# Performance work log

Hardware: AMD Instinct MI355X
Metric: run time of the kernel (lower is better)

## Reference

```python
import jax, jax.numpy as jnp
import numpy as np

TAU = 2.0        # BrainCog LIFNode default tau
THRESHOLD = 1.0
V_RESET = 0.0
HID = 512
OUT = 7
T = 16

@jax.custom_vjp
def spike(v):
    # Heaviside forward, arctan surrogate backward (BrainCog-style surrogate grad)
    return (v > 0).astype(v.dtype)

def _spike_fwd(v):
    return spike(v), v

def _spike_bwd(v, g):
    alpha = 2.0
    sg = (alpha / 2.0) / (1.0 + (jnp.pi / 2.0 * alpha * v) ** 2)
    return (g * sg,)

spike.defvjp(_spike_fwd, _spike_bwd)

def lif(mem, inp):
    # v_{t} = v_{t-1} + (I - v_{t-1}) / tau ; hard reset to v_reset=0 on spike
    v = mem + (inp - mem) / TAU
    s = spike(v - THRESHOLD)
    mem_new = v * (1.0 - jax.lax.stop_gradient(s))  # reset uses detached spike
    return mem_new, s

def setup_inputs() -> dict:
    key = jax.random.key(0)
    ks = jax.random.split(key, 9)
    B, D = 16384, 512
    sc = 0.02
    return {
        "x":     jax.random.normal(ks[0], (T, B, D), dtype=jnp.float32),
        "W_gc":  jax.random.normal(ks[1], (D, HID), dtype=jnp.float32) * sc,
        "b_gc":  jnp.zeros((HID,), jnp.float32),
        "W_pc":  jax.random.normal(ks[2], (HID, HID), dtype=jnp.float32) * sc,
        "b_pc":  jnp.zeros((HID,), jnp.float32),
        "W_d1":  jax.random.normal(ks[3], (D + HID, HID), dtype=jnp.float32) * sc,
        "b_d1":  jnp.zeros((HID,), jnp.float32),
        "W_d2":  jax.random.normal(ks[4], (HID, OUT), dtype=jnp.float32) * sc,
        "b_d2":  jnp.zeros((OUT,), jnp.float32),
    }

def reference(x, W_gc, b_gc, W_pc, b_pc, W_d1, b_d1, W_d2, b_d2):
    B = x.shape[1]
    z = jnp.zeros((B, HID), x.dtype)

    def step(carry, xt):
        m1, m2, m3 = carry
        m1, gc = lif(m1, xt @ W_gc + b_gc)                       # gc_layer
        m2, pc = lif(m2, gc @ W_pc + b_pc)                       # pc_layer
        dcn_in = jnp.concatenate([xt, pc], axis=-1)              # [B, 1024]
        m3, s3 = lif(m3, dcn_in @ W_d1 + b_d1)                   # dcn hidden LIF
        out = s3 @ W_d2 + b_d2                                   # [B, 7]
        return (m1, m2, m3), out

    _, outs = jax.lax.scan(step, (z, z, z), x)   # outs: [T, B, 7]
    return jnp.sum(outs, axis=0) / T
```

## Files before the change

### kernel.cpp

```cpp
#include <hip/hip_runtime.h>

#define TT 16
#define DD 512
#define HIDN 512
#define OUTN 7
#define NTOT 1024
#define R2 8

typedef __attribute__((ext_vector_type(8))) _Float16 half8;
typedef __attribute__((ext_vector_type(4))) _Float16 half4;
typedef __attribute__((ext_vector_type(4))) float f32x4;

#define GLD_LDS(g, l) __builtin_amdgcn_global_load_lds(                     \
    (const __attribute__((address_space(1))) void*)(g),                     \
    (__attribute__((address_space(3))) void*)(l), 16, 0, 0)

__global__ void pack_w(const float* __restrict__ Wgc, const float* __restrict__ Wd1,
                       _Float16* __restrict__ Whi, _Float16* __restrict__ Wlo)
{
    const int cell = blockIdx.x * blockDim.x + threadIdx.x;
    const int lane = cell & 63;
    const int ks   = (cell >> 6) & 15;
    const int ct   = cell >> 10;
    const float* W = (ct < 32) ? Wgc : Wd1;
    const int col  = ((ct < 32) ? ct : ct - 32) * 16 + (lane & 15);
    const int k0   = ks * 32 + ((lane >> 4) << 3);
    half8 vh, vl;
#pragma unroll
    for (int j = 0; j < 8; ++j) {
        const float w = W[(size_t)(k0 + j) * HIDN + col];
        const _Float16 h = (_Float16)w;
        vh[j] = h;
        vl[j] = (_Float16)(w - (float)h);
    }
    *reinterpret_cast<half8*>(Whi + (size_t)cell * 8) = vh;
    *reinterpret_cast<half8*>(Wlo + (size_t)cell * 8) = vl;
}

__global__ __launch_bounds__(256, 2)
void gemm_pre(const float* __restrict__ x,
              const _Float16* __restrict__ Whi, const _Float16* __restrict__ Wlo,
              float* __restrict__ G, int B, int c0, int chb)
{
    __shared__ __align__(16) _Float16 Ah[2][4096];
    __shared__ __align__(16) _Float16 Al[2][4096];
    __shared__ __align__(16) _Float16 Bh[2][4096];
    __shared__ __align__(16) _Float16 Bl[2][4096];

    const int tid  = threadIdx.x;
    const int lane = tid & 63;
    const int wave = tid >> 6;
    const int wr   = wave >> 1;
    const int wc   = wave & 1;
    const int t    = blockIdx.z;
    const size_t mrow = (size_t)blockIdx.y * 128;
    const int ct0 = blockIdx.x * 8;

    const float* xb = x + ((size_t)t * B + (size_t)c0 + mrow) * DD;
    float* Gb = G + ((size_t)t * chb + mrow) * NTOT;

    f32x4 acc[4][4];
#pragma unroll
    for (int g = 0; g < 4; ++g)
#pragma unroll
        for (int c = 0; c < 4; ++c) acc[g][c] = (f32x4){0.f, 0.f, 0.f, 0.f};

    float4 ar[4];
    const int row_u0 = tid >> 3;
    const int fg = tid & 7;

#define LOAD_A(kc)                                                            \
    {                                                                         \
        _Pragma("unroll")                                                     \
        for (int u = 0; u < 4; ++u)                                           \
            ar[u] = *reinterpret_cast<const float4*>(                         \
                xb + (size_t)(row_u0 + u * 32) * DD + (kc) * 32 + (fg << 2)); \
    }

#define CVT_WRITE(BUF)                                                        \
    {                                                                         \
        _Pragma("unroll")                                                     \
        for (int u = 0; u < 4; ++u) {                                         \
            const int row = row_u0 + u * 32;                                  \
            const int gg = row >> 4;                                          \
            const int ld = (row & 15) | ((fg >> 1) << 4);                     \
            const int offs = ((gg << 6) + ld) * 8 + ((fg & 1) << 2);          \
            const float fv[4] = {ar[u].x, ar[u].y, ar[u].z, ar[u].w};         \
            half4 vh, vl;                                                     \
            _Pragma("unroll")                                                 \
            for (int j = 0; j < 4; ++j) {                                     \
                const _Float16 h = (_Float16)fv[j];                           \
                vh[j] = h; vl[j] = (_Float16)(fv[j] - (float)h);              \
            }                                                                 \
            *reinterpret_cast<half4*>(&Ah[BUF][offs]) = vh;                   \
            *reinterpret_cast<half4*>(&Al[BUF][offs]) = vl;                   \
        }                                                                     \
    }

#define STAGE_B(kc, BUF)                                                      \
    {                                                                         \
        const int cga = wave << 1, cgb = cga + 1;                             \
        const size_t sa = ((size_t)((ct0 + cga) * 16 + (kc)) * 64 + lane) * 8;\
        const size_t sb = ((size_t)((ct0 + cgb) * 16 + (kc)) * 64 + lane) * 8;\
        GLD_LDS(Whi + sa, &Bh[BUF][cga << 9]);                                \
        GLD_LDS(Wlo + sa, &Bl[BUF][cga << 9]);                                \
        GLD_LDS(Whi + sb, &Bh[BUF][cgb << 9]);                                \
        GLD_LDS(Wlo + sb, &Bl[BUF][cgb << 9]);                                \
    }

#define COMPUTE(BUF)                                                          \
    {                                                                         \
        half8 af[4], alf[4];                                                  \
        _Pragma("unroll")                                                     \
        for (int g = 0; g < 4; ++g) {                                         \
            const int o = (((wr << 2) + g) * 64 + lane) * 8;                  \
            af[g]  = *reinterpret_cast<const half8*>(&Ah[BUF][o]);            \
            alf[g] = *reinterpret_cast<const half8*>(&Al[BUF][o]);            \
        }                                                                     \
        _Pragma("unroll")                                                     \
        for (int c = 0; c < 4; ++c) {                                         \
            const int o = (((wc << 2) + c) * 64 + lane) * 8;                  \
            const half8 bf  = *reinterpret_cast<const half8*>(&Bh[BUF][o]);   \
            const half8 blf = *reinterpret_cast<const half8*>(&Bl[BUF][o]);   \
            _Pragma("unroll")                                                 \
            for (int g = 0; g < 4; ++g) {                                     \
                acc[g][c] = __builtin_amdgcn_mfma_f32_16x16x32_f16(af[g],  bf,  acc[g][c], 0, 0, 0); \
                acc[g][c] = __builtin_amdgcn_mfma_f32_16x16x32_f16(alf[g], bf,  acc[g][c], 0, 0, 0); \
                acc[g][c] = __builtin_amdgcn_mfma_f32_16x16x32_f16(af[g],  blf, acc[g][c], 0, 0, 0); \
            }                                                                 \
        }                                                                     \
    }

    LOAD_A(0);
    STAGE_B(0, 0);
    CVT_WRITE(0);
    LOAD_A(1);
    __syncthreads();

#pragma unroll 1
    for (int kh = 0; kh < 8; ++kh) {
        CVT_WRITE(1);
        STAGE_B(2 * kh + 1, 1);
        if (2 * kh + 2 < 16) LOAD_A(2 * kh + 2);
        COMPUTE(0);
        __syncthreads();
        if (2 * kh + 2 < 16) {
            CVT_WRITE(0);
            STAGE_B(2 * kh + 2, 0);
        }
        if (2 * kh + 3 < 16) LOAD_A(2 * kh + 3);
        COMPUTE(1);
        __syncthreads();
    }

    const int r0 = (lane >> 4) << 2;
    const int cl = lane & 15;
#pragma unroll
    for (int g = 0; g < 4; ++g)
#pragma unroll
        for (int c = 0; c < 4; ++c) {
            float* gp = Gb + (size_t)((wr << 6) + (g << 4) + r0) * NTOT
                           + (blockIdx.x << 7) + (wc << 6) + (c << 4) + cl;
#pragma unroll
            for (int j = 0; j < 4; ++j) gp[(size_t)j * NTOT] = acc[g][c][j];
        }
#undef LOAD_A
#undef CVT_WRITE
#undef STAGE_B
#undef COMPUTE
}

__global__ __launch_bounds__(256, 4)
void snn_recur(const float* __restrict__ G, const float* __restrict__ bgc,
               const float* __restrict__ Wpc, const float* __restrict__ bpc,
               const float* __restrict__ Wd1, const float* __restrict__ bd1p,
               const float* __restrict__ Wd2, const float* __restrict__ bd2,
               float* __restrict__ out, int c0, int chb)
{
    __shared__ unsigned long long bits1[R2][8];
    __shared__ unsigned long long bits2[R2][8];
    __shared__ unsigned long long bits3[R2][8];
    __shared__ unsigned int rowflag[3];

    const int tid  = threadIdx.x;
    const int lane = tid & 63;
    const int wave = tid >> 6;
    const int row0l = blockIdx.x * R2;

    float m1a[R2], m1b[R2], m2a[R2], m2b[R2], m3a[R2], m3b[R2];
#pragma unroll
    for (int r = 0; r < R2; ++r) {
        m1a[r] = 0.f; m1b[r] = 0.f; m2a[r] = 0.f;
        m2b[r] = 0.f; m3a[r] = 0.f; m3b[r] = 0.f;
    }

    const float bg0 = bgc[tid],  bg1 = bgc[tid + 256];
    const float bp0 = bpc[tid],  bp1 = bpc[tid + 256];
    const float bd0 = bd1p[tid], bd1v = bd1p[tid + 256];

    float out_acc = 0.f;
    const int orow = tid / OUTN;
    const int ocol = tid - orow * OUTN;
    const bool owrite = (tid < R2 * OUTN);

    if (tid < 3) rowflag[tid] = 0u;
    __syncthreads();

#pragma unroll 1
    for (int t = 0; t < TT; ++t) {
        const float* Gt = G + ((size_t)t * chb + row0l) * NTOT;
        float ga[R2], gb[R2], g2[R2], g3[R2];
#pragma unroll
        for (int r = 0; r < R2; ++r) {
            const float* gp = Gt + (size_t)r * NTOT + tid;
            ga[r] = gp[0]; gb[r] = gp[256]; g2[r] = gp[512]; g3[r] = gp[768];
        }

#pragma unroll
        for (int r = 0; r < R2; ++r) {
            const float v0 = m1a[r] + ((ga[r] + bg0) - m1a[r]) * 0.5f;
            const bool s0 = (v0 - 1.0f) > 0.0f;
            m1a[r] = s0 ? 0.0f : v0;
            const unsigned long long k0 = __ballot(s0);
            const float v1 = m1b[r] + ((gb[r] + bg1) - m1b[r]) * 0.5f;
            const bool s1 = (v1 - 1.0f) > 0.0f;
            m1b[r] = s1 ? 0.0f : v1;
            const unsigned long long k1 = __ballot(s1);
            if (lane == 0) {
                bits1[r][wave] = k0; bits1[r][4 + wave] = k1;
                if (k0 | k1) atomicOr(&rowflag[0], 1u << r);
            }
        }
        __syncthreads();
        if (tid == 0) rowflag[2] = 0u;

        {
            const unsigned int rf = rowflag[0];
#pragma unroll
            for (int r = 0; r < R2; ++r) {
                float p0 = bp0, p1 = bp1;
                if (rf & (1u << r)) {
#pragma unroll 1
                    for (int w = 0; w < 8; ++w) {
                        unsigned long long mm = bits1[r][w];
                        while (mm) {
                            const int b = __builtin_ctzll(mm); mm &= (mm - 1);
                            const float* wp = Wpc + (size_t)((w << 6) + b) * HIDN + tid;
                            p0 += wp[0]; p1 += wp[256];
                        }
                    }
                }
                const float v0 = m2a[r] + (p0 - m2a[r]) * 0.5f;
                const bool s0 = (v0 - 1.0f) > 0.0f;
                m2a[r] = s0 ? 0.0f : v0;
                const unsigned long long k0 = __ballot(s0);
                const float v1 = m2b[r] + (p1 - m2b[r]) * 0.5f;
                const bool s1 = (v1 - 1.0f) > 0.0f;
                m2b[r] = s1 ? 0.0f : v1;
                const unsigned long long k1 = __ballot(s1);
                if (lane == 0) {
                    bits2[r][wave] = k0; bits2[r][4 + wave] = k1;
                    if (k0 | k1) atomicOr(&rowflag[1], 1u << r);
                }
            }
        }
        __syncthreads();
        if (tid == 0) rowflag[0] = 0u;

        {
            const unsigned int rf = rowflag[1];
#pragma unroll
            for (int r = 0; r < R2; ++r) {
                float p0 = g2[r] + bd0, p1 = g3[r] + bd1v;
                if (rf & (1u << r)) {
#pragma unroll 1
                    for (int w = 0; w < 8; ++w) {
                        unsigned long long mm = bits2[r][w];
                        while (mm) {
                            const int b = __builtin_ctzll(mm); mm &= (mm - 1);
                            const float* wp = Wd1 + (size_t)(DD + (w << 6) + b) * HIDN + tid;
                            p0 += wp[0]; p1 += wp[256];
                        }
                    }
                }
                const float v0 = m3a[r] + (p0 - m3a[r]) * 0.5f;
                const bool s0 = (v0 - 1.0f) > 0.0f;
                m3a[r] = s0 ? 0.0f : v0;
                const unsigned long long k0 = __ballot(s0);
                const float v1 = m3b[r] + (p1 - m3b[r]) * 0.5f;
                const bool s1 = (v1 - 1.0f) > 0.0f;
                m3b[r] = s1 ? 0.0f : v1;
                const unsigned long long k1 = __ballot(s1);
                if (lane == 0) {
                    bits3[r][wave] = k0; bits3[r][4 + wave] = k1;
                    if (k0 | k1) atomicOr(&rowflag[2], 1u << r);
                }
            }
        }
        __syncthreads();
        if (tid == 0) rowflag[1] = 0u;

        {
            const unsigned int rf = rowflag[2];
            if (owrite && (rf & (1u << orow))) {
#pragma unroll 1
                for (int w = 0; w < 8; ++w) {
                    unsigned long long mm = bits3[orow][w];
                    while (mm) {
                        const int b = __builtin_ctzll(mm); mm &= (mm - 1);
                        out_acc += Wd2[(size_t)((w << 6) + b) * OUTN + ocol];
                    }
                }
            }
        }
    }

    if (owrite)
        out[((size_t)c0 + row0l + orow) * OUTN + ocol] = out_acc * 0.0625f + bd2[ocol];
}

__global__ __launch_bounds__(256, 2)
void snn_fused_fb(const float* __restrict__ x,
                  const float* __restrict__ Wgc, const float* __restrict__ bgc,
                  const float* __restrict__ Wpc, const float* __restrict__ bpc,
                  const float* __restrict__ Wd1, const float* __restrict__ bd1p,
                  const float* __restrict__ Wd2, const float* __restrict__ bd2,
                  float* __restrict__ out, int B)
{
    __shared__ float xs[16 * DD];
    __shared__ unsigned long long bits1[16][8];
    __shared__ unsigned long long bits2[16][8];
    __shared__ unsigned long long bits3[16][8];
    __shared__ unsigned int rowflag[3];

    const int tid  = threadIdx.x;
    const int lane = tid & 63;
    const int wave = tid >> 6;
    const size_t row0 = (size_t)blockIdx.x * 16;

    float m1a[16], m1b[16], m2a[16], m2b[16], m3a[16], m3b[16];
#pragma unroll
    for (int r = 0; r < 16; ++r) {
        m1a[r] = 0.f; m1b[r] = 0.f; m2a[r] = 0.f;
        m2b[r] = 0.f; m3a[r] = 0.f; m3b[r] = 0.f;
    }

    const float bg0 = bgc[tid],  bg1 = bgc[tid + 256];
    const float bp0 = bpc[tid],  bp1 = bpc[tid + 256];
    const float bd0 = bd1p[tid], bd1 = bd1p[tid + 256];

    float out_acc = 0.f;
    const int orow = tid / OUTN;
    const int ocol = tid - orow * OUTN;
    const bool owrite = (tid < 16 * OUTN);

    if (tid < 3) rowflag[tid] = 0;
    {
        const float* src = x + row0 * DD;
#pragma unroll
        for (int u = 0; u < 8; ++u)
            GLD_LDS(src + ((u * 256 + tid) << 2), xs + ((u * 256 + wave * 64) << 2));
    }
    __syncthreads();

    for (int t = 0; t < TT; ++t) {
        float a0[16], a1[16], a2[16], a3[16];
#pragma unroll
        for (int r = 0; r < 16; ++r) { a0[r] = 0.f; a1[r] = 0.f; a2[r] = 0.f; a3[r] = 0.f; }

        const float* gp = Wgc + tid;
        const float* dp = Wd1 + tid;

        float wA0[4], wA1[4], wA2[4], wA3[4];
        float wB0[4], wB1[4], wB2[4], wB3[4];
#pragma unroll
        for (int u = 0; u < 4; ++u) {
            const size_t o = (size_t)u * HIDN;
            wA0[u] = gp[o]; wA1[u] = gp[o + 256];
            wA2[u] = dp[o]; wA3[u] = dp[o + 256];
        }
#pragma unroll 1
        for (int kk = 0; kk < DD; kk += 8) {
#pragma unroll
            for (int u = 0; u < 4; ++u) {
                const size_t o = (size_t)(kk + 4 + u) * HIDN;
                wB0[u] = gp[o]; wB1[u] = gp[o + 256];
                wB2[u] = dp[o]; wB3[u] = dp[o + 256];
            }
#pragma unroll
            for (int r = 0; r < 16; ++r) {
                const float4 xv = *reinterpret_cast<const float4*>(&xs[r * DD + kk]);
                a0[r] = fmaf(xv.x, wA0[0], a0[r]); a0[r] = fmaf(xv.y, wA0[1], a0[r]);
                a0[r] = fmaf(xv.z, wA0[2], a0[r]); a0[r] = fmaf(xv.w, wA0[3], a0[r]);
                a1[r] = fmaf(xv.x, wA1[0], a1[r]); a1[r] = fmaf(xv.y, wA1[1], a1[r]);
                a1[r] = fmaf(xv.z, wA1[2], a1[r]); a1[r] = fmaf(xv.w, wA1[3], a1[r]);
                a2[r] = fmaf(xv.x, wA2[0], a2[r]); a2[r] = fmaf(xv.y, wA2[1], a2[r]);
                a2[r] = fmaf(xv.z, wA2[2], a2[r]); a2[r] = fmaf(xv.w, wA2[3], a2[r]);
                a3[r] = fmaf(xv.x, wA3[0], a3[r]); a3[r] = fmaf(xv.y, wA3[1], a3[r]);
                a3[r] = fmaf(xv.z, wA3[2], a3[r]); a3[r] = fmaf(xv.w, wA3[3], a3[r]);
            }
            const int k2 = (kk + 8) & (DD - 1);
#pragma unroll
            for (int u = 0; u < 4; ++u) {
                const size_t o = (size_t)(k2 + u) * HIDN;
                wA0[u] = gp[o]; wA1[u] = gp[o + 256];
                wA2[u] = dp[o]; wA3[u] = dp[o + 256];
            }
#pragma unroll
            for (int r = 0; r < 16; ++r) {
                const float4 xv = *reinterpret_cast<const float4*>(&xs[r * DD + kk + 4]);
                a0[r] = fmaf(xv.x, wB0[0], a0[r]); a0[r] = fmaf(xv.y, wB0[1], a0[r]);
                a0[r] = fmaf(xv.z, wB0[2], a0[r]); a0[r] = fmaf(xv.w, wB0[3], a0[r]);
                a1[r] = fmaf(xv.x, wB1[0], a1[r]); a1[r] = fmaf(xv.y, wB1[1], a1[r]);
                a1[r] = fmaf(xv.z, wB1[2], a1[r]); a1[r] = fmaf(xv.w, wB1[3], a1[r]);
                a2[r] = fmaf(xv.x, wB2[0], a2[r]); a2[r] = fmaf(xv.y, wB2[1], a2[r]);
                a2[r] = fmaf(xv.z, wB2[2], a2[r]); a2[r] = fmaf(xv.w, wB2[3], a2[r]);
                a3[r] = fmaf(xv.x, wB3[0], a3[r]); a3[r] = fmaf(xv.y, wB3[1], a3[r]);
                a3[r] = fmaf(xv.z, wB3[2], a3[r]); a3[r] = fmaf(xv.w, wB3[3], a3[r]);
            }
        }

#pragma unroll
        for (int r = 0; r < 16; ++r) {
            const float v0 = m1a[r] + ((a0[r] + bg0) - m1a[r]) * 0.5f;
            const bool s0 = (v0 - 1.0f) > 0.0f;
            m1a[r] = s0 ? 0.0f : v0;
            const unsigned long long k0 = __ballot(s0);
            const float v1 = m1b[r] + ((a1[r] + bg1) - m1b[r]) * 0.5f;
            const bool s1 = (v1 - 1.0f) > 0.0f;
            m1b[r] = s1 ? 0.0f : v1;
            const unsigned long long k1 = __ballot(s1);
            if (lane == 0) {
                bits1[r][wave] = k0; bits1[r][4 + wave] = k1;
                if (k0 | k1) atomicOr(&rowflag[0], 1u << r);
            }
        }
        __syncthreads();

        if (tid == 0) rowflag[2] = 0;
        if (t + 1 < TT) {
            const float* src = x + (((size_t)(t + 1) * B) + row0) * DD;
#pragma unroll
            for (int u = 0; u < 8; ++u)
                GLD_LDS(src + ((u * 256 + tid) << 2), xs + ((u * 256 + wave * 64) << 2));
        }

        {
            const unsigned int rf = rowflag[0];
#pragma unroll 1
            for (int r = 0; r < 16; ++r) {
                float p0 = bp0, p1 = bp1;
                if (rf & (1u << r)) {
#pragma unroll 1
                    for (int w = 0; w < 8; ++w) {
                        unsigned long long m = bits1[r][w];
                        while (m) {
                            const int b = __builtin_ctzll(m); m &= (m - 1);
                            const float* wp = Wpc + (size_t)((w << 6) + b) * HIDN + tid;
                            p0 += wp[0]; p1 += wp[256];
                        }
                    }
                }
                const float v0 = m2a[r] + (p0 - m2a[r]) * 0.5f;
                const bool s0 = (v0 - 1.0f) > 0.0f;
                m2a[r] = s0 ? 0.0f : v0;
                const unsigned long long k0 = __ballot(s0);
                const float v1 = m2b[r] + (p1 - m2b[r]) * 0.5f;
                const bool s1 = (v1 - 1.0f) > 0.0f;
                m2b[r] = s1 ? 0.0f : v1;
                const unsigned long long k1 = __ballot(s1);
                if (lane == 0) {
                    bits2[r][wave] = k0; bits2[r][4 + wave] = k1;
                    if (k0 | k1) atomicOr(&rowflag[1], 1u << r);
                }
            }
        }
        __syncthreads();

        if (tid == 0) rowflag[0] = 0;

        {
            const unsigned int rf = rowflag[1];
#pragma unroll 1
            for (int r = 0; r < 16; ++r) {
                float p0 = a2[r] + bd0, p1 = a3[r] + bd1;
                if (rf & (1u << r)) {
#pragma unroll 1
                    for (int w = 0; w < 8; ++w) {
                        unsigned long long m = bits2[r][w];
                        while (m) {
                            const int b = __builtin_ctzll(m); m &= (m - 1);
                            const float* wp = Wd1 + (size_t)(DD + (w << 6) + b) * HIDN + tid;
                            p0 += wp[0]; p1 += wp[256];
                        }
                    }
                }
                const float v0 = m3a[r] + (p0 - m3a[r]) * 0.5f;
                const bool s0 = (v0 - 1.0f) > 0.0f;
                m3a[r] = s0 ? 0.0f : v0;
                const unsigned long long k0 = __ballot(s0);
                const float v1 = m3b[r] + (p1 - m3b[r]) * 0.5f;
                const bool s1 = (v1 - 1.0f) > 0.0f;
                m3b[r] = s1 ? 0.0f : v1;
                const unsigned long long k1 = __ballot(s1);
                if (lane == 0) {
                    bits3[r][wave] = k0; bits3[r][4 + wave] = k1;
                    if (k0 | k1) atomicOr(&rowflag[2], 1u << r);
                }
            }
        }
        __syncthreads();

        if (tid == 0) rowflag[1] = 0;

        {
            const unsigned int rf = rowflag[2];
            if (owrite && (rf & (1u << orow))) {
#pragma unroll 1
                for (int w = 0; w < 8; ++w) {
                    unsigned long long m = bits3[orow][w];
                    while (m) {
                        const int b = __builtin_ctzll(m); m &= (m - 1);
                        out_acc += Wd2[(size_t)((w << 6) + b) * OUTN + ocol];
                    }
                }
            }
        }
    }

    if (owrite) out[(row0 + orow) * OUTN + ocol] = out_acc * 0.0625f + bd2[ocol];
}

extern "C" void kernel_launch(void* const* d_in, const int* in_sizes, int n_in,
                              void* d_out, int out_size, void* d_ws, size_t ws_size,
                              hipStream_t stream) {
    const float* x   = (const float*)d_in[0];
    const float* Wgc = (const float*)d_in[1];
    const float* bgc = (const float*)d_in[2];
    const float* Wpc = (const float*)d_in[3];
    const float* bpc = (const float*)d_in[4];
    const float* Wd1 = (const float*)d_in[5];
    const float* bd1 = (const float*)d_in[6];
    const float* Wd2 = (const float*)d_in[7];
    const float* bd2 = (const float*)d_in[8];
    const int B = in_sizes[0] / (TT * DD);

    const size_t wbytes = (size_t)2 << 20;
    int chb = 4096;
    while (chb > 128 &&
           (wbytes + (size_t)TT * chb * NTOT * 4 > ws_size || (B % chb) != 0))
        chb >>= 1;
    const bool twophase =
        d_ws != nullptr &&
        ws_size >= wbytes + (size_t)TT * chb * NTOT * 4 &&
        (B % chb) == 0 && chb >= 128;

    if (!twophase) {
        hipLaunchKernelGGL(snn_fused_fb, dim3(B / 16), dim3(256), 0, stream,
                           x, Wgc, bgc, Wpc, bpc, Wd1, bd1, Wd2, bd2,
                           (float*)d_out, B);
        return;
    }

    _Float16* Whi = reinterpret_cast<_Float16*>(d_ws);
    _Float16* Wlo = Whi + 64 * 16 * 64 * 8;
    float* G = reinterpret_cast<float*>((char*)d_ws + wbytes);

    hipLaunchKernelGGL(pack_w, dim3(256), dim3(256), 0, stream, Wgc, Wd1, Whi, Wlo);

    for (int c = 0; c < B; c += chb) {
        hipLaunchKernelGGL(gemm_pre, dim3(8, chb / 128, TT), dim3(256), 0, stream,
                           x, Whi, Wlo, G, B, c, chb);
        hipLaunchKernelGGL(snn_recur, dim3(chb / R2), dim3(256), 0, stream,
                           G, bgc, Wpc, bpc, Wd1, bd1, Wd2, bd2,
                           (float*)d_out, c, chb);
    }
}
```

Before: 1.924 ms.

## Prepack x into split-fp16 MFMA layout and stream GEMM operands via global_load_lds

Adds a pack_x kernel that converts x once into hi/lo fp16 tiles already laid out for the MFMA fragments. The GEMM then stages both A and B straight into LDS with global_load_lds, so the per-tile fp32 register loads and in-kernel conversion go away. The batch-chunk loop is dropped in favour of one GEMM and one recurrence launch over the whole batch. The GEMM uses an XCD-aware 1D block mapping and nontemporal stores for G. In exchange it needs a larger workspace for the packed x and the full G, plus an extra pass over x.

```diff
diff --git a/kernel.cpp b/kernel.cpp
--- a/kernel.cpp
+++ b/kernel.cpp
@@ -8,7 +8,6 @@
 #define R2 8
 
 typedef __attribute__((ext_vector_type(8))) _Float16 half8;
-typedef __attribute__((ext_vector_type(4))) _Float16 half4;
 typedef __attribute__((ext_vector_type(4))) float f32x4;
 
 #define GLD_LDS(g, l) __builtin_amdgcn_global_load_lds(                     \
@@ -37,10 +36,45 @@
     *reinterpret_cast<half8*>(Wlo + (size_t)cell * 8) = vl;
 }
 
+__global__ void pack_x(const float* __restrict__ x,
+                       _Float16* __restrict__ Xh, _Float16* __restrict__ Xl)
+{
+    __shared__ float xs[16 * 516];
+    const int tid = threadIdx.x;
+    const size_t sub = blockIdx.x;
+    const float* src = x + sub * (16 * DD);
+#pragma unroll
+    for (int u = 0; u < 8; ++u) {
+        const int f = (u << 8) + tid;
+        const int row = f >> 7, c4 = f & 127;
+        const float4 v = *reinterpret_cast<const float4*>(src + ((size_t)f << 2));
+        *reinterpret_cast<float4*>(&xs[row * 516 + (c4 << 2)]) = v;
+    }
+    __syncthreads();
+#pragma unroll
+    for (int i = 0; i < 4; ++i) {
+        const int c = (i << 8) + tid;
+        const int ks = c >> 6, lane = c & 63;
+        const int row16 = lane & 15, kq = lane >> 4;
+        const float* p = &xs[row16 * 516 + ks * 32 + (kq << 3)];
+        half8 vh, vl;
+#pragma unroll
+        for (int j = 0; j < 8; ++j) {
+            const float f0 = p[j];
+            const _Float16 h = (_Float16)f0;
+            vh[j] = h;
+            vl[j] = (_Float16)(f0 - (float)h);
+        }
+        const size_t o = ((sub * 16 + ks) * 64 + lane) * 8;
+        *reinterpret_cast<half8*>(Xh + o) = vh;
+        *reinterpret_cast<half8*>(Xl + o) = vl;
+    }
+}
+
 __global__ __launch_bounds__(256, 2)
-void gemm_pre(const float* __restrict__ x,
+void gemm_pre(const _Float16* __restrict__ Xh, const _Float16* __restrict__ Xl,
               const _Float16* __restrict__ Whi, const _Float16* __restrict__ Wlo,
-              float* __restrict__ G, int B, int c0, int chb)
+              float* __restrict__ G, int nrt)
 {
     __shared__ __align__(16) _Float16 Ah[2][4096];
     __shared__ __align__(16) _Float16 Al[2][4096];
@@ -52,12 +86,14 @@
     const int wave = tid >> 6;
     const int wr   = wave >> 1;
     const int wc   = wave & 1;
-    const int t    = blockIdx.z;
-    const size_t mrow = (size_t)blockIdx.y * 128;
-    const int ct0 = blockIdx.x * 8;
-
-    const float* xb = x + ((size_t)t * B + (size_t)c0 + mrow) * DD;
-    float* Gb = G + ((size_t)t * chb + mrow) * NTOT;
+
+    const int disp = blockIdx.x;
+    const int xcd  = disp & 7;
+    const int q    = disp >> 3;
+    const int rt   = xcd * (nrt >> 3) + (q >> 3);
+    const int ct0  = (q & 7) << 3;
+
+    const int g0 = wave << 1, g1 = g0 + 1;
 
     f32x4 acc[4][4];
 #pragma unroll
@@ -65,47 +101,20 @@
 #pragma unroll
         for (int c = 0; c < 4; ++c) acc[g][c] = (f32x4){0.f, 0.f, 0.f, 0.f};
 
-    float4 ar[4];
-    const int row_u0 = tid >> 3;
-    const int fg = tid & 7;
-
-#define LOAD_A(kc)                                                            \
+#define STAGE(kc, BUF)                                                        \
     {                                                                         \
-        _Pragma("unroll")                                                     \
-        for (int u = 0; u < 4; ++u)                                           \
-            ar[u] = *reinterpret_cast<const float4*>(                         \
-                xb + (size_t)(row_u0 + u * 32) * DD + (kc) * 32 + (fg << 2)); \
-    }
-
-#define CVT_WRITE(BUF)                                                        \
-    {                                                                         \
-        _Pragma("unroll")                                                     \
-        for (int u = 0; u < 4; ++u) {                                         \
-            const int row = row_u0 + u * 32;                                  \
-            const int gg = row >> 4;                                          \
-            const int ld = (row & 15) | ((fg >> 1) << 4);                     \
-            const int offs = ((gg << 6) + ld) * 8 + ((fg & 1) << 2);          \
-            const float fv[4] = {ar[u].x, ar[u].y, ar[u].z, ar[u].w};         \
-            half4 vh, vl;                                                     \
-            _Pragma("unroll")                                                 \
-            for (int j = 0; j < 4; ++j) {                                     \
-                const _Float16 h = (_Float16)fv[j];                           \
-                vh[j] = h; vl[j] = (_Float16)(fv[j] - (float)h);              \
-            }                                                                 \
-            *reinterpret_cast<half4*>(&Ah[BUF][offs]) = vh;                   \
-            *reinterpret_cast<half4*>(&Al[BUF][offs]) = vl;                   \
-        }                                                                     \
-    }
-
-#define STAGE_B(kc, BUF)                                                      \
-    {                                                                         \
-        const int cga = wave << 1, cgb = cga + 1;                             \
-        const size_t sa = ((size_t)((ct0 + cga) * 16 + (kc)) * 64 + lane) * 8;\
-        const size_t sb = ((size_t)((ct0 + cgb) * 16 + (kc)) * 64 + lane) * 8;\
-        GLD_LDS(Whi + sa, &Bh[BUF][cga << 9]);                                \
-        GLD_LDS(Wlo + sa, &Bl[BUF][cga << 9]);                                \
-        GLD_LDS(Whi + sb, &Bh[BUF][cgb << 9]);                                \
-        GLD_LDS(Wlo + sb, &Bl[BUF][cgb << 9]);                                \
+        const size_t sa0 = (((size_t)(rt * 8 + g0) * 16 + (kc)) * 64 + lane) * 8; \
+        const size_t sa1 = (((size_t)(rt * 8 + g1) * 16 + (kc)) * 64 + lane) * 8; \
+        GLD_LDS(Xh + sa0, &Ah[BUF][g0 << 9]);                                 \
+        GLD_LDS(Xl + sa0, &Al[BUF][g0 << 9]);                                 \
+        GLD_LDS(Xh + sa1, &Ah[BUF][g1 << 9]);                                 \
+        GLD_LDS(Xl + sa1, &Al[BUF][g1 << 9]);                                 \
+        const size_t sb0 = (((size_t)(ct0 + g0) * 16 + (kc)) * 64 + lane) * 8;\
+        const size_t sb1 = (((size_t)(ct0 + g1) * 16 + (kc)) * 64 + lane) * 8;\
+        GLD_LDS(Whi + sb0, &Bh[BUF][g0 << 9]);                                \
+        GLD_LDS(Wlo + sb0, &Bl[BUF][g0 << 9]);                                \
+        GLD_LDS(Whi + sb1, &Bh[BUF][g1 << 9]);                                \
+        GLD_LDS(Wlo + sb1, &Bl[BUF][g1 << 9]);                                \
     }
 
 #define COMPUTE(BUF)                                                          \
@@ -131,42 +140,33 @@
         }                                                                     \
     }
 
-    LOAD_A(0);
-    STAGE_B(0, 0);
-    CVT_WRITE(0);
-    LOAD_A(1);
+    STAGE(0, 0);
     __syncthreads();
 
 #pragma unroll 1
     for (int kh = 0; kh < 8; ++kh) {
-        CVT_WRITE(1);
-        STAGE_B(2 * kh + 1, 1);
-        if (2 * kh + 2 < 16) LOAD_A(2 * kh + 2);
+        STAGE(2 * kh + 1, 1);
         COMPUTE(0);
         __syncthreads();
-        if (2 * kh + 2 < 16) {
-            CVT_WRITE(0);
-            STAGE_B(2 * kh + 2, 0);
-        }
-        if (2 * kh + 3 < 16) LOAD_A(2 * kh + 3);
+        if (2 * kh + 2 < 16) STAGE(2 * kh + 2, 0);
         COMPUTE(1);
         __syncthreads();
     }
 
     const int r0 = (lane >> 4) << 2;
     const int cl = lane & 15;
+    const size_t m0 = (size_t)rt << 7;
 #pragma unroll
     for (int g = 0; g < 4; ++g)
 #pragma unroll
         for (int c = 0; c < 4; ++c) {
-            float* gp = Gb + (size_t)((wr << 6) + (g << 4) + r0) * NTOT
-                           + (blockIdx.x << 7) + (wc << 6) + (c << 4) + cl;
-#pragma unroll
-            for (int j = 0; j < 4; ++j) gp[(size_t)j * NTOT] = acc[g][c][j];
-        }
-#undef LOAD_A
-#undef CVT_WRITE
-#undef STAGE_B
+            float* gp = G + (m0 + (size_t)((wr << 6) + (g << 4) + r0)) * NTOT
+                          + (ct0 << 4) + (wc << 6) + (c << 4) + cl;
+#pragma unroll
+            for (int j = 0; j < 4; ++j)
+                __builtin_nontemporal_store(acc[g][c][j], gp + (size_t)j * NTOT);
+        }
+#undef STAGE
 #undef COMPUTE
 }
 
@@ -175,7 +175,7 @@
                const float* __restrict__ Wpc, const float* __restrict__ bpc,
                const float* __restrict__ Wd1, const float* __restrict__ bd1p,
                const float* __restrict__ Wd2, const float* __restrict__ bd2,
-               float* __restrict__ out, int c0, int chb)
+               float* __restrict__ out, int Btot)
 {
     __shared__ unsigned long long bits1[R2][8];
     __shared__ unsigned long long bits2[R2][8];
@@ -208,7 +208,7 @@
 
 #pragma unroll 1
     for (int t = 0; t < TT; ++t) {
-        const float* Gt = G + ((size_t)t * chb + row0l) * NTOT;
+        const float* Gt = G + ((size_t)t * Btot + row0l) * NTOT;
         float ga[R2], gb[R2], g2[R2], g3[R2];
 #pragma unroll
         for (int r = 0; r < R2; ++r) {
@@ -316,7 +316,7 @@
     }
 
     if (owrite)
-        out[((size_t)c0 + row0l + orow) * OUTN + ocol] = out_acc * 0.0625f + bd2[ocol];
+        out[(size_t)(row0l + orow) * OUTN + ocol] = out_acc * 0.0625f + bd2[ocol];
 }
 
 __global__ __launch_bounds__(256, 2)
@@ -545,17 +545,16 @@
     const float* bd2 = (const float*)d_in[8];
     const int B = in_sizes[0] / (TT * DD);
 
-    const size_t wbytes = (size_t)2 << 20;
-    int chb = 4096;
-    while (chb > 128 &&
-           (wbytes + (size_t)TT * chb * NTOT * 4 > ws_size || (B % chb) != 0))
-        chb >>= 1;
-    const bool twophase =
-        d_ws != nullptr &&
-        ws_size >= wbytes + (size_t)TT * chb * NTOT * 4 &&
-        (B % chb) == 0 && chb >= 128;
-
-    if (!twophase) {
+    const size_t MB = (size_t)1 << 20;
+    const size_t xp_bytes = (size_t)TT * B * DD * 2;
+    const size_t g_bytes  = (size_t)TT * B * NTOT * 4;
+    const size_t need = 2 * MB + 2 * xp_bytes + g_bytes;
+    const int nrt = (TT * B) / 128;
+
+    const bool ok = d_ws != nullptr && ws_size >= need &&
+                    (B % 128) == 0 && (nrt % 8) == 0 && (B % R2) == 0;
+
+    if (!ok) {
         hipLaunchKernelGGL(snn_fused_fb, dim3(B / 16), dim3(256), 0, stream,
                            x, Wgc, bgc, Wpc, bpc, Wd1, bd1, Wd2, bd2,
                            (float*)d_out, B);
@@ -563,16 +562,16 @@
     }
 
     _Float16* Whi = reinterpret_cast<_Float16*>(d_ws);
-    _Float16* Wlo = Whi + 64 * 16 * 64 * 8;
-    float* G = reinterpret_cast<float*>((char*)d_ws + wbytes);
+    _Float16* Wlo = Whi + (size_t)64 * 16 * 64 * 8;
+    _Float16* Xh  = reinterpret_cast<_Float16*>((char*)d_ws + 2 * MB);
+    _Float16* Xl  = Xh + (size_t)TT * B * DD;
+    float*    G   = reinterpret_cast<float*>((char*)d_ws + 2 * MB + 2 * xp_bytes);
 
     hipLaunchKernelGGL(pack_w, dim3(256), dim3(256), 0, stream, Wgc, Wd1, Whi, Wlo);
-
-    for (int c = 0; c < B; c += chb) {
-        hipLaunchKernelGGL(gemm_pre, dim3(8, chb / 128, TT), dim3(256), 0, stream,
-                           x, Whi, Wlo, G, B, c, chb);
-        hipLaunchKernelGGL(snn_recur, dim3(chb / R2), dim3(256), 0, stream,
-                           G, bgc, Wpc, bpc, Wd1, bd1, Wd2, bd2,
-                           (float*)d_out, c, chb);
-    }
+    hipLaunchKernelGGL(pack_x, dim3((TT * B) / 16), dim3(256), 0, stream, x, Xh, Xl);
+    hipLaunchKernelGGL(gemm_pre, dim3(nrt * 8), dim3(256), 0, stream,
+                       Xh, Xl, Whi, Wlo, G, nrt);
+    hipLaunchKernelGGL(snn_recur, dim3(B / R2), dim3(256), 0, stream,
+                       G, bgc, Wpc, bpc, Wd1, bd1, Wd2, bd2,
+                       (float*)d_out, B);
 }
```

After: 1.957 ms. Within noise of the previous version (+1.7%).
